# Performance work log

Hardware: AMD Instinct MI355X
Metric: run time of the kernel (lower is better)

The kernel has to match this reference:

```python
import jax, jax.numpy as jnp
import numpy as np

SIZE = (256, 256, 256)   # volume shape (self.size)
N = 65536                # number of Gaussians
DIST = 3.0               # render cutoff distance
WIN = 7                  # static stencil width = 2*ceil(DIST)+1


def setup_inputs() -> dict:
    key = jax.random.key(0)
    k1, k2, k3 = jax.random.split(key, 3)
    # positions inside the volume
    pos = jax.random.uniform(k1, (3, N), minval=1.0, maxval=255.0)
    # per-Gaussian value
    value = jax.random.uniform(k2, (1, N), minval=0.1, maxval=1.0)
    # radii: diagonal radii in [1,3], off-diagonal cross terms ~ 0 (1e-5, as in create_guass)
    rdiag = jax.random.uniform(k3, (3, N), minval=1.0, maxval=3.0)
    off = jnp.full((N,), 1e-5, jnp.float32)
    # layout rows 4:10 -> [rx, rxy, rxz, ry, ryz, rz]
    r = jnp.stack([rdiag[0], off, off, rdiag[1], off, rdiag[2]], axis=0)
    paras = jnp.concatenate([pos, value, r], axis=0)  # [10, N]
    return {
        "paras": paras,
        "distance": jnp.float32(DIST),
        "thredhold": jnp.float32(1e-4),
    }


def _render(paras, distance, thredhold):
    # paras: [10, N] -> position [3,N], value [N], r [6,N]
    pos = paras[:3]
    val = paras[3]
    r = paras[4:]
    D0, D1, D2 = SIZE
    size_arr = jnp.array(SIZE, jnp.int32)

    # static local stencil offsets [W^3, 3]
    offs = jnp.stack(
        jnp.meshgrid(jnp.arange(WIN), jnp.arange(WIN), jnp.arange(WIN), indexing="ij"),
        axis=-1,
    ).reshape(-1, 3).astype(jnp.int32)

    corner = jnp.floor(pos.T).astype(jnp.int32) - (WIN // 2)   # [N, 3]
    vox = corner[:, None, :] + offs[None, :, :]                 # [N, W^3, 3] voxel coords
    d = vox.astype(paras.dtype) - pos.T[:, None, :]             # [N, W^3, 3] voxel - center
    dx, dy, dz = d[..., 0], d[..., 1], d[..., 2]

    rx, rxy, rxz, ry, ryz, rz = r  # each [N]
    # anisotropic quadratic form: diagonal radii + cross terms
    q = (
        (dx / rx[:, None]) ** 2
        + (dy / ry[:, None]) ** 2
        + (dz / rz[:, None]) ** 2
        + rxy[:, None] * dx * dy
        + rxz[:, None] * dx * dz
        + ryz[:, None] * dy * dz
    )
    w = jnp.exp(-0.5 * q)                                       # [N, W^3]

    dist2 = dx * dx + dy * dy + dz * dz
    inb = jnp.all((vox >= 0) & (vox < size_arr), axis=-1)
    mask = inb & (dist2 <= distance * distance) & (w > thredhold)
    contrib = jnp.where(mask, val[:, None] * w, 0.0)

    voxc = jnp.clip(vox, 0, size_arr - 1)
    flat = (voxc[..., 0] * D1 + voxc[..., 1]) * D2 + voxc[..., 2]
    out = jnp.zeros(D0 * D1 * D2, paras.dtype).at[flat.reshape(-1)].add(contrib.reshape(-1))
    return out.reshape(SIZE)


def reference(paras, distance, thredhold):
    return _render(paras, distance, thredhold)
```

## Files before the change

kernel.cpp:

```cpp
#include <hip/hip_runtime.h>

#define D0 256
#define D1 256
#define D2 256
#define NPTS 65536
#define HALF 3

#define TX 32
#define TY 16
#define TZ 16
#define NTILES 2048
#define TILE_VOX (TX * TY * TZ)

#define BLK 512
#define WPB 8
#define CAP 256
#define CSTRIDE 16

#define WS_COUNTS 0
#define WS_PREP   (NTILES * CSTRIDE)
#define WS_LIST   (WS_PREP + NPTS * 12)
#define LIST_INTS (NTILES * CAP / 2)
#define FULL_INTS  (WS_LIST + LIST_INTS)
#define WS_LIST_NP (NTILES * CSTRIDE)
#define SMALL_INTS (WS_LIST_NP + LIST_INTS)

struct OffTable { unsigned v[256]; };

constexpr OffTable make_table() {
    OffTable t{};
    int m[7] = {9, 4, 1, 0, 0, 1, 4};
    int n = 0;
    for (int i = 0; i < 7; i++)
        for (int j = 0; j < 7; j++)
            for (int k = 0; k < 7; k++)
                if (m[i] + m[j] + m[k] <= 9)
                    t.v[n++] = (unsigned)(i | (j << 8) | (k << 16));
    for (; n < 256; n++)
        t.v[n] = (unsigned)(100 | (100 << 8) | (100 << 16));
    return t;
}

__device__ __constant__ OffTable g_tab = make_table();

struct PP { float fx, fy, fz, val, ix, iy, iz, D, E, F; int pack; };

template<bool PREP>
__device__ __forceinline__ PP load_pt(const float* __restrict__ paras,
                                      const float* __restrict__ prep, int pidx) {
    PP P;
    if constexpr (PREP) {
        const float4* p4 = (const float4*)prep + pidx * 3;
        float4 a = p4[0], b4 = p4[1], c4 = p4[2];
        P.fx = a.x;  P.fy = a.y;  P.fz = a.z;  P.val = a.w;
        P.ix = b4.x; P.iy = b4.y; P.iz = b4.z; P.D = b4.w;
        P.E = c4.x;  P.F = c4.y;  P.pack = __float_as_int(c4.z);
    } else {
        float px = paras[pidx], py = paras[NPTS + pidx], pz = paras[2 * NPTS + pidx];
        P.val = paras[3 * NPTS + pidx];
        float rx  = paras[4 * NPTS + pidx], rxy = paras[5 * NPTS + pidx];
        float rxz = paras[6 * NPTS + pidx], ry  = paras[7 * NPTS + pidx];
        float ryz = paras[8 * NPTS + pidx], rz  = paras[9 * NPTS + pidx];
        int cx = (int)floorf(px) - HALF;
        int cy = (int)floorf(py) - HALF;
        int cz = (int)floorf(pz) - HALF;
        P.fx = (float)cx - px; P.fy = (float)cy - py; P.fz = (float)cz - pz;
        P.ix = __fdividef(1.f, rx); P.iy = __fdividef(1.f, ry);
        P.iz = __fdividef(1.f, rz);
        P.D = rxy; P.E = rxz; P.F = ryz;
        P.pack = (cx + 8) | ((cy + 8) << 10) | ((cz + 8) << 20);
    }
    return P;
}

__global__ __launch_bounds__(256)
void bin_kernel(const float* __restrict__ paras, int* __restrict__ ws,
                float* __restrict__ prep, int do_prep, int list_off) {
    int t = blockIdx.x * 256 + threadIdx.x;
    int p = t >> 3, j = t & 7;

    float px = paras[p], py = paras[NPTS + p], pz = paras[2 * NPTS + p];
    int cx = (int)floorf(px) - HALF;
    int cy = (int)floorf(py) - HALF;
    int cz = (int)floorf(pz) - HALF;

    if (do_prep && j == 0) {
        float val = paras[3 * NPTS + p];
        float rx  = paras[4 * NPTS + p], rxy = paras[5 * NPTS + p];
        float rxz = paras[6 * NPTS + p], ry  = paras[7 * NPTS + p];
        float ryz = paras[8 * NPTS + p], rz  = paras[9 * NPTS + p];
        int pack = (cx + 8) | ((cy + 8) << 10) | ((cz + 8) << 20);
        float4* o = (float4*)prep + p * 3;
        o[0] = make_float4((float)cx - px, (float)cy - py, (float)cz - pz, val);
        o[1] = make_float4(__fdividef(1.f, rx), __fdividef(1.f, ry),
                           __fdividef(1.f, rz), rxy);
        o[2] = make_float4(rxz, ryz, __int_as_float(pack), 0.f);
    }

    int xlo = max(cx, 0), xhi = min(cx + 6, D0 - 1);
    int ylo = max(cy, 0), yhi = min(cy + 6, D1 - 1);
    int zlo = max(cz, 0), zhi = min(cz + 6, D2 - 1);
    int txa = xlo >> 5, txb = xhi >> 5;
    int tya = ylo >> 4, tyb = yhi >> 4;
    int tza = zlo >> 4, tzb = zhi >> 4;

    bool dup = ((j & 1) && txb == txa) ||
               ((j & 2) && tyb == tya) ||
               ((j & 4) && tzb == tza);
    if (!dup) {
        int tx = (j & 1) ? txb : txa;
        int ty = (j & 2) ? tyb : tya;
        int tz = (j & 4) ? tzb : tza;
        int tt = (tx << 8) | (ty << 4) | tz;
        int slot = atomicAdd(&ws[WS_COUNTS + tt * CSTRIDE], 1);
        if (slot < CAP)
            ((unsigned short*)(ws + list_off))[tt * CAP + slot] = (unsigned short)p;
    }
}

template<bool PREP>
__global__ __launch_bounds__(512)
void tile_splat(const float* __restrict__ paras,
                const float* __restrict__ prep,
                const float* __restrict__ dist_p,
                const float* __restrict__ thr_p,
                const int* __restrict__ ws, int list_off,
                float* __restrict__ out) {
    __shared__ float acc[TILE_VOX];

    const int b   = blockIdx.x;
    const int tzi = b & 15, tyi = (b >> 4) & 15, txi = b >> 8;
    const int X0 = txi * TX, Y0 = tyi * TY, Z0 = tzi * TZ;
    const int tid = threadIdx.x;
    const int wid = tid >> 6, lane = tid & 63;

    int   oiv[4], ojv[4], okv[4];
    float foi[4], foj[4], fok[4];
#pragma unroll
    for (int t = 0; t < 4; t++) {
        unsigned pk = g_tab.v[t * 64 + lane];
        oiv[t] = pk & 255; ojv[t] = (pk >> 8) & 255; okv[t] = (int)(pk >> 16);
        foi[t] = (float)oiv[t]; foj[t] = (float)ojv[t]; fok[t] = (float)okv[t];
    }

    float4* acc4 = (float4*)acc;
    for (int q = tid; q < TILE_VOX / 4; q += BLK)
        acc4[q] = make_float4(0.f, 0.f, 0.f, 0.f);
    __syncthreads();

    const int n = min(ws[WS_COUNTS + b * CSTRIDE], CAP);
    const unsigned short* list = (const unsigned short*)(ws + list_off) + b * CAP;
    const float dist  = dist_p[0];
    const float thr   = thr_p[0];
    const float d2max = dist * dist;

    int i = wid;
    PP cur;
    if (i < n) {
        int pidx = __builtin_amdgcn_readfirstlane((int)list[i]);
        cur = load_pt<PREP>(paras, prep, pidx);
    }
    while (i < n) {
        int inext = i + WPB;
        PP nxt = cur;
        if (inext < n) {
            int pidx2 = __builtin_amdgcn_readfirstlane((int)list[inext]);
            nxt = load_pt<PREP>(paras, prep, pidx2);
        }

        int pk  = cur.pack;
        int vx0 = (pk & 1023) - 8 - X0;
        int vy0 = ((pk >> 10) & 1023) - 8 - Y0;
        int vz0 = (pk >> 20) - 8 - Z0;

#pragma unroll
        for (int t = 0; t < 4; t++) {
            int vx = vx0 + oiv[t], vy = vy0 + ojv[t], vz = vz0 + okv[t];
            float dx = cur.fx + foi[t];
            float dy = cur.fy + foj[t];
            float dz = cur.fz + fok[t];
            float d2 = dx * dx + dy * dy + dz * dz;

            bool pass = ((unsigned)vx < (unsigned)TX) &
                        ((unsigned)vy < (unsigned)TY) &
                        ((unsigned)vz < (unsigned)TZ) &
                        (d2 <= d2max);
            if (pass) {
                float ax = dx * cur.ix, ay = dy * cur.iy, az = dz * cur.iz;
                float q = ax * ax + ay * ay + az * az
                        + cur.D * dx * dy + cur.E * dx * dz + cur.F * dy * dz;
                float w = __expf(-0.5f * q);
                if (w > thr)
                    atomicAdd(&acc[(vx << 8) | (vy << 4) | vz], cur.val * w);
            }
        }
        cur = nxt;
        i = inext;
    }
    __syncthreads();

    for (int q = tid; q < TILE_VOX / 4; q += BLK) {
        int vz = (q & 3) << 2;
        int vy = (q >> 2) & 15;
        int vx = q >> 6;
        *(float4*)&out[((X0 + vx) * D1 + (Y0 + vy)) * D2 + Z0 + vz] = acc4[q];
    }
}

__global__ __launch_bounds__(256)
void zero_kernel(float4* __restrict__ out, int n4) {
    int i = blockIdx.x * blockDim.x + threadIdx.x;
    int stride = gridDim.x * blockDim.x;
    for (; i < n4; i += stride)
        out[i] = make_float4(0.f, 0.f, 0.f, 0.f);
}

__global__ __launch_bounds__(256)
void splat_fallback(const float* __restrict__ paras,
                    const float* __restrict__ dist_p,
                    const float* __restrict__ thr_p,
                    float* __restrict__ out) {
    int wave = (blockIdx.x * blockDim.x + threadIdx.x) >> 6;
    int lane = threadIdx.x & 63;
    int p = __builtin_amdgcn_readfirstlane(wave);

    const int N = NPTS;
    float px  = paras[0 * N + p], py  = paras[1 * N + p], pz  = paras[2 * N + p];
    float val = paras[3 * N + p];
    float rx  = paras[4 * N + p], rxy = paras[5 * N + p], rxz = paras[6 * N + p];
    float ry  = paras[7 * N + p], ryz = paras[8 * N + p], rz  = paras[9 * N + p];

    float dist = dist_p[0], thr = thr_p[0];
    float d2max = dist * dist;

    int cx = (int)floorf(px) - HALF;
    int cy = (int)floorf(py) - HALF;
    int cz = (int)floorf(pz) - HALF;
    float fx = (float)cx - px, fy = (float)cy - py, fz = (float)cz - pz;
    float irx = __fdividef(1.f, rx), iry = __fdividef(1.f, ry),
          irz = __fdividef(1.f, rz);

#pragma unroll
    for (int t = 0; t < 4; t++) {
        unsigned pk = g_tab.v[t * 64 + lane];
        int oi = pk & 255, oj = (pk >> 8) & 255, ok = pk >> 16;
        int vx = cx + oi, vy = cy + oj, vz = cz + ok;
        float dx = fx + (float)oi, dy = fy + (float)oj, dz = fz + (float)ok;
        float d2 = dx * dx + dy * dy + dz * dz;
        bool inb = ((unsigned)vx < (unsigned)D0) &
                   ((unsigned)vy < (unsigned)D1) &
                   ((unsigned)vz < (unsigned)D2);
        if (inb && d2 <= d2max) {
            float ax = dx * irx, ay = dy * iry, az = dz * irz;
            float q = ax * ax + ay * ay + az * az
                    + rxy * dx * dy + rxz * dx * dz + ryz * dy * dz;
            float w = __expf(-0.5f * q);
            if (w > thr)
                atomicAdd(&out[(vx << 16) + (vy << 8) + vz], val * w);
        }
    }
}

extern "C" void kernel_launch(void* const* d_in, const int* in_sizes, int n_in,
                              void* d_out, int out_size, void* d_ws, size_t ws_size,
                              hipStream_t stream) {
    const float* paras  = (const float*)d_in[0];
    const float* dist_p = (const float*)d_in[1];
    const float* thr_p  = (const float*)d_in[2];
    float* out = (float*)d_out;
    int* ws = (int*)d_ws;
    float* prep = (float*)(ws + WS_PREP);

    if (ws_size >= (size_t)FULL_INTS * 4) {
        hipMemsetAsync(ws, 0, NTILES * CSTRIDE * sizeof(int), stream);
        bin_kernel<<<NPTS * 8 / 256, 256, 0, stream>>>(paras, ws, prep, 1, WS_LIST);
        tile_splat<true><<<NTILES, BLK, 0, stream>>>(paras, prep, dist_p, thr_p,
                                                     ws, WS_LIST, out);
    } else if (ws_size >= (size_t)SMALL_INTS * 4) {
        hipMemsetAsync(ws, 0, NTILES * CSTRIDE * sizeof(int), stream);
        bin_kernel<<<NPTS * 8 / 256, 256, 0, stream>>>(paras, ws, prep, 0, WS_LIST_NP);
        tile_splat<false><<<NTILES, BLK, 0, stream>>>(paras, prep, dist_p, thr_p,
                                                      ws, WS_LIST_NP, out);
    } else {
        zero_kernel<<<4096, 256, 0, stream>>>((float4*)out, out_size / 4);
        splat_fallback<<<NPTS / 4, 256, 0, stream>>>(paras, dist_p, thr_p, out);
    }
}
```

Baseline: 130.9 us.

## Fuse binning and tile splat into one kernel with grid barrier

Merges the binning kernel and the tile splat kernel into one persistent launch of 1024 blocks. A global atomic barrier separates the binning phase from the splat phase, and each block then processes two tiles in turn. The goal is to remove a kernel launch and the gap between kernels. The cost is a spin barrier that needs all 1024 blocks resident at once, otherwise it deadlocks. It also halves the tile-level parallelism available for load balancing.

```diff
diff --git a/kernel.cpp b/kernel.cpp
--- a/kernel.cpp
+++ b/kernel.cpp
@@ -14,15 +14,17 @@
 
 #define BLK 512
 #define WPB 8
+#define NBLK 1024
 #define CAP 256
 #define CSTRIDE 16
 
-#define WS_COUNTS 0
-#define WS_PREP   (NTILES * CSTRIDE)
+#define WS_BAR    0
+#define WS_COUNTS 16
+#define WS_PREP   (WS_COUNTS + NTILES * CSTRIDE)
 #define WS_LIST   (WS_PREP + NPTS * 12)
 #define LIST_INTS (NTILES * CAP / 2)
 #define FULL_INTS  (WS_LIST + LIST_INTS)
-#define WS_LIST_NP (NTILES * CSTRIDE)
+#define WS_LIST_NP WS_PREP
 #define SMALL_INTS (WS_LIST_NP + LIST_INTS)
 
 struct OffTable { unsigned v[256]; };
@@ -73,69 +75,72 @@
     return P;
 }
 
-__global__ __launch_bounds__(256)
-void bin_kernel(const float* __restrict__ paras, int* __restrict__ ws,
-                float* __restrict__ prep, int do_prep, int list_off) {
-    int t = blockIdx.x * 256 + threadIdx.x;
-    int p = t >> 3, j = t & 7;
-
-    float px = paras[p], py = paras[NPTS + p], pz = paras[2 * NPTS + p];
-    int cx = (int)floorf(px) - HALF;
-    int cy = (int)floorf(py) - HALF;
-    int cz = (int)floorf(pz) - HALF;
-
-    if (do_prep && j == 0) {
-        float val = paras[3 * NPTS + p];
-        float rx  = paras[4 * NPTS + p], rxy = paras[5 * NPTS + p];
-        float rxz = paras[6 * NPTS + p], ry  = paras[7 * NPTS + p];
-        float ryz = paras[8 * NPTS + p], rz  = paras[9 * NPTS + p];
-        int pack = (cx + 8) | ((cy + 8) << 10) | ((cz + 8) << 20);
-        float4* o = (float4*)prep + p * 3;
-        o[0] = make_float4((float)cx - px, (float)cy - py, (float)cz - pz, val);
-        o[1] = make_float4(__fdividef(1.f, rx), __fdividef(1.f, ry),
-                           __fdividef(1.f, rz), rxy);
-        o[2] = make_float4(rxz, ryz, __int_as_float(pack), 0.f);
-    }
-
-    int xlo = max(cx, 0), xhi = min(cx + 6, D0 - 1);
-    int ylo = max(cy, 0), yhi = min(cy + 6, D1 - 1);
-    int zlo = max(cz, 0), zhi = min(cz + 6, D2 - 1);
-    int txa = xlo >> 5, txb = xhi >> 5;
-    int tya = ylo >> 4, tyb = yhi >> 4;
-    int tza = zlo >> 4, tzb = zhi >> 4;
-
-    bool dup = ((j & 1) && txb == txa) ||
-               ((j & 2) && tyb == tya) ||
-               ((j & 4) && tzb == tza);
-    if (!dup) {
-        int tx = (j & 1) ? txb : txa;
-        int ty = (j & 2) ? tyb : tya;
-        int tz = (j & 4) ? tzb : tza;
-        int tt = (tx << 8) | (ty << 4) | tz;
-        int slot = atomicAdd(&ws[WS_COUNTS + tt * CSTRIDE], 1);
-        if (slot < CAP)
-            ((unsigned short*)(ws + list_off))[tt * CAP + slot] = (unsigned short)p;
-    }
-}
-
 template<bool PREP>
-__global__ __launch_bounds__(512)
-void tile_splat(const float* __restrict__ paras,
-                const float* __restrict__ prep,
-                const float* __restrict__ dist_p,
-                const float* __restrict__ thr_p,
-                const int* __restrict__ ws, int list_off,
-                float* __restrict__ out) {
+__global__ __launch_bounds__(512, 8)
+void fused_splat(const float* __restrict__ paras,
+                 const float* __restrict__ dist_p,
+                 const float* __restrict__ thr_p,
+                 int* __restrict__ ws, int list_off,
+                 float* __restrict__ out) {
     __shared__ float acc[TILE_VOX];
 
-    const int b   = blockIdx.x;
-    const int tzi = b & 15, tyi = (b >> 4) & 15, txi = b >> 8;
-    const int X0 = txi * TX, Y0 = tyi * TY, Z0 = tzi * TZ;
-    const int tid = threadIdx.x;
-    const int wid = tid >> 6, lane = tid & 63;
+    const int tid  = threadIdx.x;
+    const int gtid = blockIdx.x * BLK + tid;
+
+    {
+        int p = gtid >> 3, j = gtid & 7;
+        float px = paras[p], py = paras[NPTS + p], pz = paras[2 * NPTS + p];
+        int cx = (int)floorf(px) - HALF;
+        int cy = (int)floorf(py) - HALF;
+        int cz = (int)floorf(pz) - HALF;
+
+        if (PREP && j == 0) {
+            float val = paras[3 * NPTS + p];
+            float rx  = paras[4 * NPTS + p], rxy = paras[5 * NPTS + p];
+            float rxz = paras[6 * NPTS + p], ry  = paras[7 * NPTS + p];
+            float ryz = paras[8 * NPTS + p], rz  = paras[9 * NPTS + p];
+            int pack = (cx + 8) | ((cy + 8) << 10) | ((cz + 8) << 20);
+            float4* o = (float4*)(ws + WS_PREP) + p * 3;
+            o[0] = make_float4((float)cx - px, (float)cy - py, (float)cz - pz, val);
+            o[1] = make_float4(__fdividef(1.f, rx), __fdividef(1.f, ry),
+                               __fdividef(1.f, rz), rxy);
+            o[2] = make_float4(rxz, ryz, __int_as_float(pack), 0.f);
+        }
+
+        int xlo = max(cx, 0), xhi = min(cx + 6, D0 - 1);
+        int ylo = max(cy, 0), yhi = min(cy + 6, D1 - 1);
+        int zlo = max(cz, 0), zhi = min(cz + 6, D2 - 1);
+        int txa = xlo >> 5, txb = xhi >> 5;
+        int tya = ylo >> 4, tyb = yhi >> 4;
+        int tza = zlo >> 4, tzb = zhi >> 4;
+
+        bool dup = ((j & 1) && txb == txa) ||
+                   ((j & 2) && tyb == tya) ||
+                   ((j & 4) && tzb == tza);
+        if (!dup) {
+            int tx = (j & 1) ? txb : txa;
+            int ty = (j & 2) ? tyb : tya;
+            int tz = (j & 4) ? tzb : tza;
+            int tt = (tx << 8) | (ty << 4) | tz;
+            int slot = atomicAdd(&ws[WS_COUNTS + tt * CSTRIDE], 1);
+            if (slot < CAP)
+                ((unsigned short*)(ws + list_off))[tt * CAP + slot] = (unsigned short)p;
+        }
+    }
+
+    __syncthreads();
+    if (tid == 0) {
+        __hip_atomic_fetch_add(&ws[WS_BAR], 1, __ATOMIC_ACQ_REL,
+                               __HIP_MEMORY_SCOPE_AGENT);
+        while (__hip_atomic_load(&ws[WS_BAR], __ATOMIC_ACQUIRE,
+                                 __HIP_MEMORY_SCOPE_AGENT) < NBLK)
+            __builtin_amdgcn_s_sleep(2);
+    }
+    __syncthreads();
 
     int   oiv[4], ojv[4], okv[4];
     float foi[4], foj[4], fok[4];
+    const int lane = tid & 63, wid = tid >> 6;
 #pragma unroll
     for (int t = 0; t < 4; t++) {
         unsigned pk = g_tab.v[t * 64 + lane];
@@ -143,67 +148,76 @@
         foi[t] = (float)oiv[t]; foj[t] = (float)ojv[t]; fok[t] = (float)okv[t];
     }
 
-    float4* acc4 = (float4*)acc;
-    for (int q = tid; q < TILE_VOX / 4; q += BLK)
-        acc4[q] = make_float4(0.f, 0.f, 0.f, 0.f);
-    __syncthreads();
-
-    const int n = min(ws[WS_COUNTS + b * CSTRIDE], CAP);
-    const unsigned short* list = (const unsigned short*)(ws + list_off) + b * CAP;
     const float dist  = dist_p[0];
     const float thr   = thr_p[0];
     const float d2max = dist * dist;
-
-    int i = wid;
-    PP cur;
-    if (i < n) {
-        int pidx = __builtin_amdgcn_readfirstlane((int)list[i]);
-        cur = load_pt<PREP>(paras, prep, pidx);
-    }
-    while (i < n) {
-        int inext = i + WPB;
-        PP nxt = cur;
-        if (inext < n) {
-            int pidx2 = __builtin_amdgcn_readfirstlane((int)list[inext]);
-            nxt = load_pt<PREP>(paras, prep, pidx2);
-        }
-
-        int pk  = cur.pack;
-        int vx0 = (pk & 1023) - 8 - X0;
-        int vy0 = ((pk >> 10) & 1023) - 8 - Y0;
-        int vz0 = (pk >> 20) - 8 - Z0;
+    float4* acc4 = (float4*)acc;
+
+    for (int rep = 0; rep < 2; rep++) {
+        const int b = (blockIdx.x << 1) | rep;
+        const int tzi = b & 15, tyi = (b >> 4) & 15, txi = b >> 8;
+        const int X0 = txi * TX, Y0 = tyi * TY, Z0 = tzi * TZ;
+
+        for (int q = tid; q < TILE_VOX / 4; q += BLK)
+            acc4[q] = make_float4(0.f, 0.f, 0.f, 0.f);
+        __syncthreads();
+
+        const int n = min(ws[WS_COUNTS + b * CSTRIDE], CAP);
+        const unsigned short* list =
+            (const unsigned short*)(ws + list_off) + b * CAP;
+
+        int i = wid;
+        PP cur;
+        if (i < n) {
+            int pidx = __builtin_amdgcn_readfirstlane((int)list[i]);
+            cur = load_pt<PREP>(paras, (const float*)(ws + WS_PREP), pidx);
+        }
+        while (i < n) {
+            int inext = i + WPB;
+            PP nxt = cur;
+            if (inext < n) {
+                int pidx2 = __builtin_amdgcn_readfirstlane((int)list[inext]);
+                nxt = load_pt<PREP>(paras, (const float*)(ws + WS_PREP), pidx2);
+            }
+
+            int pk  = cur.pack;
+            int vx0 = (pk & 1023) - 8 - X0;
+            int vy0 = ((pk >> 10) & 1023) - 8 - Y0;
+            int vz0 = (pk >> 20) - 8 - Z0;
 
 #pragma unroll
-        for (int t = 0; t < 4; t++) {
-            int vx = vx0 + oiv[t], vy = vy0 + ojv[t], vz = vz0 + okv[t];
-            float dx = cur.fx + foi[t];
-            float dy = cur.fy + foj[t];
-            float dz = cur.fz + fok[t];
-            float d2 = dx * dx + dy * dy + dz * dz;
-
-            bool pass = ((unsigned)vx < (unsigned)TX) &
-                        ((unsigned)vy < (unsigned)TY) &
-                        ((unsigned)vz < (unsigned)TZ) &
-                        (d2 <= d2max);
-            if (pass) {
-                float ax = dx * cur.ix, ay = dy * cur.iy, az = dz * cur.iz;
-                float q = ax * ax + ay * ay + az * az
-                        + cur.D * dx * dy + cur.E * dx * dz + cur.F * dy * dz;
-                float w = __expf(-0.5f * q);
-                if (w > thr)
-                    atomicAdd(&acc[(vx << 8) | (vy << 4) | vz], cur.val * w);
+            for (int t = 0; t < 4; t++) {
+                int vx = vx0 + oiv[t], vy = vy0 + ojv[t], vz = vz0 + okv[t];
+                float dx = cur.fx + foi[t];
+                float dy = cur.fy + foj[t];
+                float dz = cur.fz + fok[t];
+                float d2 = dx * dx + dy * dy + dz * dz;
+
+                bool pass = ((unsigned)vx < (unsigned)TX) &
+                            ((unsigned)vy < (unsigned)TY) &
+                            ((unsigned)vz < (unsigned)TZ) &
+                            (d2 <= d2max);
+                if (pass) {
+                    float ax = dx * cur.ix, ay = dy * cur.iy, az = dz * cur.iz;
+                    float q = ax * ax + ay * ay + az * az
+                            + cur.D * dx * dy + cur.E * dx * dz + cur.F * dy * dz;
+                    float w = __expf(-0.5f * q);
+                    if (w > thr)
+                        atomicAdd(&acc[(vx << 8) | (vy << 4) | vz], cur.val * w);
+                }
             }
-        }
-        cur = nxt;
-        i = inext;
-    }
-    __syncthreads();
-
-    for (int q = tid; q < TILE_VOX / 4; q += BLK) {
-        int vz = (q & 3) << 2;
-        int vy = (q >> 2) & 15;
-        int vx = q >> 6;
-        *(float4*)&out[((X0 + vx) * D1 + (Y0 + vy)) * D2 + Z0 + vz] = acc4[q];
+            cur = nxt;
+            i = inext;
+        }
+        __syncthreads();
+
+        for (int q = tid; q < TILE_VOX / 4; q += BLK) {
+            int vz = (q & 3) << 2;
+            int vy = (q >> 2) & 15;
+            int vx = q >> 6;
+            *(float4*)&out[((X0 + vx) * D1 + (Y0 + vy)) * D2 + Z0 + vz] = acc4[q];
+        }
+        __syncthreads();
     }
 }
 
@@ -269,18 +283,15 @@
     const float* thr_p  = (const float*)d_in[2];
     float* out = (float*)d_out;
     int* ws = (int*)d_ws;
-    float* prep = (float*)(ws + WS_PREP);
 
     if (ws_size >= (size_t)FULL_INTS * 4) {
-        hipMemsetAsync(ws, 0, NTILES * CSTRIDE * sizeof(int), stream);
-        bin_kernel<<<NPTS * 8 / 256, 256, 0, stream>>>(paras, ws, prep, 1, WS_LIST);
-        tile_splat<true><<<NTILES, BLK, 0, stream>>>(paras, prep, dist_p, thr_p,
-                                                     ws, WS_LIST, out);
+        hipMemsetAsync(ws, 0, (size_t)(WS_COUNTS + NTILES * CSTRIDE) * 4, stream);
+        fused_splat<true><<<NBLK, BLK, 0, stream>>>(paras, dist_p, thr_p,
+                                                    ws, WS_LIST, out);
     } else if (ws_size >= (size_t)SMALL_INTS * 4) {
-        hipMemsetAsync(ws, 0, NTILES * CSTRIDE * sizeof(int), stream);
-        bin_kernel<<<NPTS * 8 / 256, 256, 0, stream>>>(paras, ws, prep, 0, WS_LIST_NP);
-        tile_splat<false><<<NTILES, BLK, 0, stream>>>(paras, prep, dist_p, thr_p,
-                                                      ws, WS_LIST_NP, out);
+        hipMemsetAsync(ws, 0, (size_t)(WS_COUNTS + NTILES * CSTRIDE) * 4, stream);
+        fused_splat<false><<<NBLK, BLK, 0, stream>>>(paras, dist_p, thr_p,
+                                                     ws, WS_LIST_NP, out);
     } else {
         zero_kernel<<<4096, 256, 0, stream>>>((float4*)out, out_size / 4);
         splat_fallback<<<NPTS / 4, 256, 0, stream>>>(paras, dist_p, thr_p, out);
```

Result: slower. 243.8 us (+86.3%).
